# Optimization experiments

Measured on AMD Instinct MI355X. Metric: run time of the kernel, lower is better.

Reference implementation:

```python
import jax, jax.numpy as jnp
import numpy as np

N_NODES = 50000
N_EDGES = 800000
D = 64
N_LAYERS = 5
N_GRAPHS = 256
N_CLASSES = 10
BN_EPS = 1e-5


def setup_inputs() -> dict:
    key = jax.random.key(0)
    ks = jax.random.split(key, 16)
    s = 1.0 / np.sqrt(D)
    return {
        "X": jax.random.normal(ks[0], (N_NODES, D), jnp.float32),
        "edge_index": jax.random.randint(ks[1], (2, N_EDGES), 0, N_NODES, jnp.int64),
        "batch": jnp.sort(jax.random.randint(ks[2], (N_NODES,), 0, N_GRAPHS, jnp.int64)),
        "Wk": jax.random.normal(ks[3], (N_LAYERS, D, D), jnp.float32) * s,
        "Wq": jax.random.normal(ks[4], (N_LAYERS, D, D), jnp.float32) * s,
        "Wv": jax.random.normal(ks[5], (N_LAYERS, D, D), jnp.float32) * s,
        "Ws": jax.random.normal(ks[6], (N_LAYERS, D, D), jnp.float32) * s,
        "bk": jnp.zeros((N_LAYERS, D), jnp.float32),
        "bq": jnp.zeros((N_LAYERS, D), jnp.float32),
        "bv": jnp.zeros((N_LAYERS, D), jnp.float32),
        "bconv": jnp.zeros((N_LAYERS, D), jnp.float32),
        "gamma": jnp.ones((N_LAYERS, D), jnp.float32),
        "beta": jnp.zeros((N_LAYERS, D), jnp.float32),
        "Wlin": jax.random.normal(ks[7], (D, N_CLASSES), jnp.float32) * s,
        "blin": jnp.zeros((N_CLASSES,), jnp.float32),
    }


def _res_gated_conv(x, src, dst, Wk, Wq, Wv, Ws, bk, bq, bv, b):
    # PyG ResGatedGraphConv: out_i = W_skip x_i + b + sum_{j->i} sigmoid(K x_i + Q x_j) * (V x_j)
    k = x @ Wk + bk  # [N, D]
    q = x @ Wq + bq
    v = x @ Wv + bv
    eta = jax.nn.sigmoid(k[dst] + q[src])         # [E, D] gate
    agg = jax.ops.segment_sum(eta * v[src], dst, num_segments=x.shape[0])
    return agg + x @ Ws + b


def _batch_norm(x, gamma, beta):
    mean = jnp.mean(x, axis=0)
    var = jnp.mean(jnp.square(x - mean), axis=0)  # biased, as torch BN training
    return (x - mean) * jax.lax.rsqrt(var + BN_EPS) * gamma + beta


def reference(X, edge_index, batch, Wk, Wq, Wv, Ws, bk, bq, bv, bconv, gamma, beta, Wlin, blin):
    src, dst = edge_index[0], edge_index[1]
    h = X
    for l in range(N_LAYERS):  # dropout_prob = 0 -> dropout is identity
        h = _res_gated_conv(h, src, dst, Wk[l], Wq[l], Wv[l], Ws[l], bk[l], bq[l], bv[l], bconv[l])
        h = jax.nn.relu(h)
        h = _batch_norm(h, gamma[l], beta[l])
    # global mean pool over graphs
    sums = jax.ops.segment_sum(h, batch, num_segments=N_GRAPHS)
    counts = jax.ops.segment_sum(jnp.ones((h.shape[0], 1), h.dtype), batch, num_segments=N_GRAPHS)
    pooled = sums / jnp.maximum(counts, 1.0)
    logits = pooled @ Wlin + blin
    return jax.nn.softmax(logits, axis=-1)
```

## Files before the change

### kernel.cpp

```cpp
#include <hip/hip_runtime.h>

#define NN 50000
#define NE 800000
#define DD 64
#define NL 5
#define NG 256
#define NC 10
#define BN_EPS 1e-5f
#define NCHUNK ((NN + 255) / 256)
#define GROWS 64
#define GT (GROWS / 16)
#define SAW 68
#define GEMM_BLOCKS ((NN + GROWS - 1) / GROWS)
#define NNS (NN + 8)
#define PADDEG(d) (((d) + 7) & ~7)
#define DEG_BLOCKS ((NE + 255) / 256)
#define WPREP_BLOCKS ((NL * 2048 + 255) / 256)
#define FCHK 2048
#define FCHUNKS ((NE + FCHK - 1) / FCHK)
#define FILLP_BLOCKS (8 * FCHUNKS)
#define NRANGE (NN / 8)
#define PAD_BLOCKS NCHUNK
#define L2E 1.4426950408889634f

typedef __attribute__((ext_vector_type(8))) short bf16x8;
typedef __attribute__((ext_vector_type(4))) float f32x4;

__device__ inline float bf2f(unsigned short u) {
    return __uint_as_float((unsigned)u << 16);
}
__device__ inline unsigned short f2bf(float x) {
    unsigned u = __float_as_uint(x);
    u += 0x7FFFu + ((u >> 16) & 1u);
    return (unsigned short)(u >> 16);
}

__device__ inline unsigned int pack_bf16x2(float a, float b) {
    unsigned int ua = __float_as_uint(a);
    unsigned int ub = __float_as_uint(b);
    ua += 0x7FFFu + ((ua >> 16) & 1u);
    ub += 0x7FFFu + ((ub >> 16) & 1u);
    return (ub & 0xFFFF0000u) | (ua >> 16);
}

__device__ inline void split_bf16(float x, short& h, short& l) {
    const unsigned u  = __float_as_uint(x);
    const unsigned hb = u & 0xFFFF0000u;
    h = (short)(hb >> 16);
    const float lo = x - __uint_as_float(hb);
    l = (short)(__float_as_uint(lo) >> 16);
}

__device__ inline float p_eq(unsigned p) { return __uint_as_float(p << 16); }
__device__ inline float p_v(unsigned p)  { return __uint_as_float(p & 0xFFFF0000u); }

#define GPAIR(ek, pa, pb, acc) { \
    const float t1_ = fmaf(ek, p_eq(pa), 1.f); \
    const float t2_ = fmaf(ek, p_eq(pb), 1.f); \
    const float R_  = __builtin_amdgcn_rcpf(t1_ * t2_); \
    acc = fmaf(fmaf(p_v(pb), t1_, p_v(pa) * t2_), R_, acc); }

#define GCOLS(ekx, eky, p, accx, accy) { \
    const float t1_ = fmaf(ekx, p_eq(p.x), 1.f); \
    const float t2_ = fmaf(eky, p_eq(p.y), 1.f); \
    const float R_  = __builtin_amdgcn_rcpf(t1_ * t2_); \
    accx = fmaf(p_v(p.x), R_ * t2_, accx); \
    accy = fmaf(p_v(p.y), R_ * t1_, accy); }

template<int F32>
__device__ __forceinline__ void gemm_body(
    const void* __restrict__ HinV,
    const bf16x8* __restrict__ whbuf, const bf16x8* __restrict__ wlbuf,
    const float* __restrict__ bk, const float* __restrict__ bq,
    const float* __restrict__ bv, const float* __restrict__ bs,
    const float* __restrict__ prevStats,
    const float* __restrict__ prevGamma, const float* __restrict__ prevBeta,
    unsigned short* __restrict__ Kq, unsigned int* __restrict__ QVq,
    unsigned short* __restrict__ Hq, const int gb)
{
    __shared__ unsigned int sA[GROWS * SAW];
    __shared__ float sAB[128];
    const int tid = threadIdx.x;

    if (!F32) {
        if (tid < 64) {
            const float invN = 1.0f / (float)NN;
            const float mean = prevStats[tid] * invN;
            const float var  = prevStats[64 + tid] * invN - mean * mean;
            const float inv  = rsqrtf(var + BN_EPS);
            const float a = inv * prevGamma[tid];
            sAB[tid]      = a;
            sAB[64 + tid] = prevBeta[tid] - mean * a;
        }
        __syncthreads();
    }

    const int row0 = gb * GROWS;
    if (F32) {
        const float* X = (const float*)HinV;
        for (int i = tid; i < GROWS * 16; i += 256) {
            const int row = i >> 4;
            const int k4  = (i & 15) * 4;
            float4 x = make_float4(0.f, 0.f, 0.f, 0.f);
            if (row0 + row < NN)
                x = *(const float4*)(X + (size_t)(row0 + row) * DD + k4);
            const float xs[4] = {x.x, x.y, x.z, x.w};
            unsigned int* dst = &sA[row * SAW + k4];
#pragma unroll
            for (int j = 0; j < 4; j++) {
                short hs, ls;
                split_bf16(xs[j], hs, ls);
                dst[j] = ((unsigned int)(unsigned short)hs << 16) | (unsigned short)ls;
            }
        }
    } else {
        const unsigned short* Hin = (const unsigned short*)HinV;
        for (int i = tid; i < GROWS * 8; i += 256) {
            const int row = i >> 3;
            const int cb  = (i & 7) * 8;
            const int q   = cb >> 4;
            const int o16 = cb & 15;
            uint4 v = make_uint4(0u, 0u, 0u, 0u);
            if (row0 + row < NN)
                v = *(const uint4*)&Hin[((size_t)q * NN + row0 + row) * 16 + o16];
            const unsigned ws[4] = {v.x, v.y, v.z, v.w};
            unsigned int* dst = &sA[row * SAW + cb];
#pragma unroll
            for (int j = 0; j < 4; j++) {
                const float x0 = bf2f((unsigned short)(ws[j] & 0xFFFFu));
                const float x1 = bf2f((unsigned short)(ws[j] >> 16));
                const int c0 = cb + 2 * j, c1 = cb + 2 * j + 1;
                short hs, ls;
                split_bf16(fmaf(x0, sAB[c0], sAB[64 + c0]), hs, ls);
                dst[2 * j] = ((unsigned int)(unsigned short)hs << 16) | (unsigned short)ls;
                split_bf16(fmaf(x1, sAB[c1], sAB[64 + c1]), hs, ls);
                dst[2 * j + 1] = ((unsigned int)(unsigned short)hs << 16) | (unsigned short)ls;
            }
        }
    }

    const int wave = tid >> 6;
    const int lane = tid & 63;
    const int n15  = lane & 15;
    const int g    = lane >> 4;
    const int col  = wave * 16 + n15;

    bf16x8 wh[4][2], wl[4][2];
    {
        const int base = wave * 64 + lane;
#pragma unroll
        for (int m = 0; m < 4; m++)
#pragma unroll
            for (int c = 0; c < 2; c++) {
                const int idx = m * 512 + c * 256 + base;
                wh[m][c] = whbuf[idx];
                wl[m][c] = wlbuf[idx];
            }
    }

    const float nbk = -bk[col] * L2E;
    const float nbq = -bq[col] * L2E;
    const float bvc = bv[col], bsc = bs[col];
    __syncthreads();

#pragma unroll 1
    for (int t = 0; t < GT; t++) {
        const int rowbase = row0 + t * 16;
        if (rowbase >= NN) break;

        bf16x8 ah[2], al[2];
#pragma unroll
        for (int c = 0; c < 2; c++) {
            const uint4 u0 = *(const uint4*)&sA[(t * 16 + n15) * SAW + g * 8 + 32 * c];
            const uint4 u1 = *(const uint4*)&sA[(t * 16 + n15) * SAW + g * 8 + 32 * c + 4];
            const unsigned int us[8] = {u0.x, u0.y, u0.z, u0.w, u1.x, u1.y, u1.z, u1.w};
            bf16x8 h, l;
#pragma unroll
            for (int j = 0; j < 8; j++) {
                h[j] = (short)(us[j] >> 16);
                l[j] = (short)(us[j] & 0xFFFFu);
            }
            ah[c] = h; al[c] = l;
        }

        f32x4 acc[4];
#pragma unroll
        for (int m = 0; m < 4; m++) acc[m] = (f32x4){0.f, 0.f, 0.f, 0.f};

#pragma unroll
        for (int c = 0; c < 2; c++) {
#pragma unroll
            for (int m = 0; m < 4; m++) {
                acc[m] = __builtin_amdgcn_mfma_f32_16x16x32_bf16(ah[c], wh[m][c], acc[m], 0, 0, 0);
                acc[m] = __builtin_amdgcn_mfma_f32_16x16x32_bf16(al[c], wh[m][c], acc[m], 0, 0, 0);
                acc[m] = __builtin_amdgcn_mfma_f32_16x16x32_bf16(ah[c], wl[m][c], acc[m], 0, 0, 0);
            }
        }

#pragma unroll
        for (int r = 0; r < 4; r++) {
            const int row = rowbase + g * 4 + r;
            const size_t o  = ((size_t)wave * NN  + row) * 16 + n15;
            const size_t oq = ((size_t)wave * NNS + row) * 16 + n15;
            Kq[o]   = f2bf(__builtin_amdgcn_exp2f(fmaf(acc[0][r], -L2E, nbk)));
            QVq[oq] = pack_bf16x2(__builtin_amdgcn_exp2f(fmaf(acc[1][r], -L2E, nbq)),
                                  acc[2][r] + bvc);
            Hq[o]   = f2bf(acc[3][r] + bsc);
        }
    }
}

__global__ __launch_bounds__(256) void prep_kernel(
    const int* __restrict__ ei, int* __restrict__ deg,
    const float* __restrict__ Wk, const float* __restrict__ Wq,
    const float* __restrict__ Wv, const float* __restrict__ Ws,
    bf16x8* __restrict__ whbuf, bf16x8* __restrict__ wlbuf,
    unsigned int* __restrict__ QVq)
{
    const int bid = blockIdx.x;
    if (bid < DEG_BLOCKS) {
        const int e = bid * 256 + threadIdx.x;
        if (e < NE) atomicAdd(&deg[ei[NE + e]], 1);
        return;
    }
    if (bid == DEG_BLOCKS && threadIdx.x < 64) {
        const int q = threadIdx.x >> 4, c = threadIdx.x & 15;
        QVq[((size_t)q * NNS + NN) * 16 + c] = 0u;
    }
    const int t = (bid - DEG_BLOCKS) * 256 + threadIdx.x;
    if (t >= NL * 2048) return;
    const int lane = t & 63;
    const int w    = (t >> 6) & 3;
    const int c    = (t >> 8) & 1;
    const int m    = (t >> 9) & 3;
    const int l    = t >> 11;

    const float* Wm4[4] = {Wk, Wq, Wv, Ws};
    const float* W = Wm4[m] + l * 4096;
    const int col = w * 16 + (lane & 15);
    const int g   = lane >> 4;

    bf16x8 h, lo;
#pragma unroll
    for (int j = 0; j < 8; j++) {
        const int k = g * 8 + j + 32 * c;
        short hs, ls;
        split_bf16(W[k * DD + col], hs, ls);
        h[j] = hs; lo[j] = ls;
    }
    whbuf[t] = h;
    wlbuf[t] = lo;
}

__global__ __launch_bounds__(256) void scan_partial_kernel(
    const int* __restrict__ deg, int* __restrict__ psums)
{
    __shared__ int ls[256];
    const int i = blockIdx.x * 256 + threadIdx.x;
    ls[threadIdx.x] = (i < NN) ? PADDEG(deg[i]) : 0;
    __syncthreads();
    for (int off = 128; off > 0; off >>= 1) {
        if (threadIdx.x < off) ls[threadIdx.x] += ls[threadIdx.x + off];
        __syncthreads();
    }
    if (threadIdx.x == 0) psums[blockIdx.x] = ls[0];
}

__global__ __launch_bounds__(64) void scan_offsets_kernel(
    int* __restrict__ psums, int* __restrict__ rowst)
{
    const int lane = threadIdx.x;
    const int base = lane * 4;
    int v[4];
    int s = 0;
#pragma unroll
    for (int j = 0; j < 4; j++) {
        v[j] = (base + j < NCHUNK) ? psums[base + j] : 0;
        s += v[j];
    }
    int incl = s;
    for (int off = 1; off < 64; off <<= 1) {
        const int t = __shfl_up(incl, off);
        if (lane >= off) incl += t;
    }
    const int total = __shfl(incl, 63);
    int run = incl - s;
#pragma unroll
    for (int j = 0; j < 4; j++) {
        if (base + j < NCHUNK) psums[base + j] = run;
        run += v[j];
    }
    if (lane == 0) rowst[NN] = total;
}

__global__ __launch_bounds__(256) void scan_final_kernel(
    const int* __restrict__ deg, const int* __restrict__ psums,
    int* __restrict__ rowst, int* __restrict__ cursor)
{
    __shared__ int ls[256];
    const int i = blockIdx.x * 256 + threadIdx.x;
    const int x = (i < NN) ? PADDEG(deg[i]) : 0;
    ls[threadIdx.x] = x;
    __syncthreads();
    for (int off = 1; off < 256; off <<= 1) {
        int v = (threadIdx.x >= off) ? ls[threadIdx.x - off] : 0;
        __syncthreads();
        ls[threadIdx.x] += v;
        __syncthreads();
    }
    if (i < NN) {
        const int excl = psums[blockIdx.x] + ls[threadIdx.x] - x;
        rowst[i]  = excl;
        cursor[i] = excl;
    }
}

__global__ __launch_bounds__(256) void gfp_kernel(
    const float* __restrict__ X,
    const bf16x8* __restrict__ whbuf, const bf16x8* __restrict__ wlbuf,
    const float* __restrict__ bk, const float* __restrict__ bq,
    const float* __restrict__ bv, const float* __restrict__ bs,
    unsigned short* __restrict__ Kq, unsigned int* __restrict__ QVq,
    unsigned short* __restrict__ Hq,
    const int* __restrict__ ei, int* __restrict__ cursor,
    const int* __restrict__ rowst, const int* __restrict__ deg,
    unsigned short* __restrict__ csr16)
{
    const int bid = blockIdx.x;
    if (bid < GEMM_BLOCKS) {
        gemm_body<1>(X, whbuf, wlbuf, bk, bq, bv, bs,
                     nullptr, nullptr, nullptr, Kq, QVq, Hq, bid);
        return;
    }
    if (bid < GEMM_BLOCKS + FILLP_BLOCKS) {
        const int fid = bid - GEMM_BLOCKS;
        const int r   = bid & 7;
        const int o   = fid >> 3;
        const int lo  = r * NRANGE;
        const int hi  = lo + NRANGE;
        const int e0  = o * FCHK;
        const int e1  = min(e0 + FCHK, NE);
        for (int e = e0 + threadIdx.x; e < e1; e += 256) {
            const int dst = ei[NE + e];
            if (dst >= lo && dst < hi) {
                const int src = ei[e];
                csr16[atomicAdd(&cursor[dst], 1)] = (unsigned short)src;
            }
        }
        return;
    }
    const int n = (bid - GEMM_BLOCKS - FILLP_BLOCKS) * 256 + threadIdx.x;
    if (n >= NN) return;
    const int end = rowst[n + 1];
    for (int i = rowst[n] + deg[n]; i < end; i++) csr16[i] = (unsigned short)NN;
}

__global__ __launch_bounds__(256) void gemm4_mfma(
    const void* __restrict__ HinV,
    const bf16x8* __restrict__ whbuf, const bf16x8* __restrict__ wlbuf,
    const float* __restrict__ bk, const float* __restrict__ bq,
    const float* __restrict__ bv, const float* __restrict__ bs,
    const float* __restrict__ prevStats,
    const float* __restrict__ prevGamma, const float* __restrict__ prevBeta,
    unsigned short* __restrict__ Kq, unsigned int* __restrict__ QVq,
    unsigned short* __restrict__ Hq)
{
    gemm_body<0>(HinV, whbuf, wlbuf, bk, bq, bv, bs,
                 prevStats, prevGamma, prevBeta, Kq, QVq, Hq, blockIdx.x);
}

#define GATHER_BLOCKS (8 * 782)
__global__ __launch_bounds__(256) void gather_kernel(
    const int* __restrict__ rowst, const unsigned short* __restrict__ csr16,
    const unsigned short* __restrict__ Kq, const unsigned int* __restrict__ QVq,
    unsigned short* Hq, float* __restrict__ stats)
{
    const int tid  = threadIdx.x;
    const int wv   = tid >> 6;
    const int lane = tid & 63;
    const int eoff = lane >> 3;
    const int cp   = lane & 7;

    const int j       = blockIdx.x;
    const int xcd     = j & 7;
    const int quarter = xcd >> 1;
    const int half    = xcd & 1;
    const int nodebase = ((j >> 3) * 2 + half) * 32 + wv * 8;

    const unsigned* Kq32 = (const unsigned*)(Kq + (size_t)quarter * NN * 16);
    const uint2*    Qq2  = (const uint2*)(QVq + (size_t)quarter * NNS * 16);
    unsigned*       Hq32 = (unsigned*)(Hq + (size_t)quarter * NN * 16);

    float se = 0.f, s2e = 0.f, so = 0.f, s2o = 0.f;

    int e00 = __builtin_amdgcn_readfirstlane(rowst[min(nodebase, NN)]);

    for (int t = 0; t < 4; t++) {
        const int n0 = nodebase + 2 * t;
        if (n0 >= NN) break;
        const int n1 = n0 + 1;
        const unsigned ho0 = (unsigned)(n0 * 8 + cp);
        const unsigned ho1 = (unsigned)(n1 * 8 + cp);
        unsigned h0p = 0u, h1p = 0u;
        if (eoff == 0) {
            h0p = Hq32[ho0];
            h1p = Hq32[ho1];
        }
        const unsigned k0p = Kq32[ho0];
        const unsigned k1p = Kq32[ho1];
        const float ek00 = bf2f((unsigned short)(k0p & 0xFFFFu));
        const float ek01 = bf2f((unsigned short)(k0p >> 16));
        const float ek10 = bf2f((unsigned short)(k1p & 0xFFFFu));
        const float ek11 = bf2f((unsigned short)(k1p >> 16));
        const int e01 = __builtin_amdgcn_readfirstlane(rowst[n1]);
        const int e11 = __builtin_amdgcn_readfirstlane(rowst[n1 + 1]);
        int nd0 = (e01 - e00) >> 3;
        int nd1 = (e11 - e01) >> 3;
        int ndm = min(nd0, nd1);
        nd0 -= ndm; nd1 -= ndm;
        int b0 = e00, b1 = e01;
        e00 = e11;
        float a00 = 0.f, a01 = 0.f, a10 = 0.f, a11 = 0.f;

        while (ndm >= 2) {
            const unsigned s0 = *(const unsigned*)(csr16 + b0 + 2 * eoff);
            const unsigned s1 = *(const unsigned*)(csr16 + b1 + 2 * eoff);
            const uint2 p0a = Qq2[(s0 & 0xFFFFu) * 8u + cp];
            const uint2 p0b = Qq2[(s0 >> 16) * 8u + cp];
            const uint2 p1a = Qq2[(s1 & 0xFFFFu) * 8u + cp];
            const uint2 p1b = Qq2[(s1 >> 16) * 8u + cp];
            GPAIR(ek00, p0a.x, p0b.x, a00);
            GPAIR(ek01, p0a.y, p0b.y, a01);
            GPAIR(ek10, p1a.x, p1b.x, a10);
            GPAIR(ek11, p1a.y, p1b.y, a11);
            b0 += 16; b1 += 16; ndm -= 2;
        }
        if (ndm) {
            const int s0 = csr16[b0 + eoff];
            const int s1 = csr16[b1 + eoff];
            const uint2 p0 = Qq2[(unsigned)(s0 * 8 + cp)];
            const uint2 p1 = Qq2[(unsigned)(s1 * 8 + cp)];
            GCOLS(ek00, ek01, p0, a00, a01);
            GCOLS(ek10, ek11, p1, a10, a11);
            b0 += 8; b1 += 8;
        }
        while (nd0 >= 2) {
            const unsigned s0 = *(const unsigned*)(csr16 + b0 + 2 * eoff);
            const uint2 p0a = Qq2[(s0 & 0xFFFFu) * 8u + cp];
            const uint2 p0b = Qq2[(s0 >> 16) * 8u + cp];
            GPAIR(ek00, p0a.x, p0b.x, a00);
            GPAIR(ek01, p0a.y, p0b.y, a01);
            b0 += 16; nd0 -= 2;
        }
        if (nd0) {
            const int s0 = csr16[b0 + eoff];
            const uint2 p0 = Qq2[(unsigned)(s0 * 8 + cp)];
            GCOLS(ek00, ek01, p0, a00, a01);
        }
        while (nd1 >= 2) {
            const unsigned s1 = *(const unsigned*)(csr16 + b1 + 2 * eoff);
            const uint2 p1a = Qq2[(s1 & 0xFFFFu) * 8u + cp];
            const uint2 p1b = Qq2[(s1 >> 16) * 8u + cp];
            GPAIR(ek10, p1a.x, p1b.x, a10);
            GPAIR(ek11, p1a.y, p1b.y, a11);
            b1 += 16; nd1 -= 2;
        }
        if (nd1) {
            const int s1 = csr16[b1 + eoff];
            const uint2 p1 = Qq2[(unsigned)(s1 * 8 + cp)];
            GCOLS(ek10, ek11, p1, a10, a11);
        }

        a00 += __shfl_xor(a00, 8);  a00 += __shfl_xor(a00, 16); a00 += __shfl_xor(a00, 32);
        a01 += __shfl_xor(a01, 8);  a01 += __shfl_xor(a01, 16); a01 += __shfl_xor(a01, 32);
        a10 += __shfl_xor(a10, 8);  a10 += __shfl_xor(a10, 16); a10 += __shfl_xor(a10, 32);
        a11 += __shfl_xor(a11, 8);  a11 += __shfl_xor(a11, 16); a11 += __shfl_xor(a11, 32);

        if (eoff == 0) {
            const float o00 = fmaxf(bf2f((unsigned short)(h0p & 0xFFFFu)) + a00, 0.f);
            const float o01 = fmaxf(bf2f((unsigned short)(h0p >> 16))     + a01, 0.f);
            const float o10 = fmaxf(bf2f((unsigned short)(h1p & 0xFFFFu)) + a10, 0.f);
            const float o11 = fmaxf(bf2f((unsigned short)(h1p >> 16))     + a11, 0.f);
            const unsigned short b00 = f2bf(o00), b01 = f2bf(o01);
            const unsigned short b10 = f2bf(o10), b11 = f2bf(o11);
            Hq32[ho0] = ((unsigned)b01 << 16) | b00;
            Hq32[ho1] = ((unsigned)b11 << 16) | b10;
            const float r00 = bf2f(b00), r01 = bf2f(b01);
            const float r10 = bf2f(b10), r11 = bf2f(b11);
            se  += r00 + r10;  s2e += r00 * r00 + r10 * r10;
            so  += r01 + r11;  s2o += r01 * r01 + r11 * r11;
        }
    }

    __shared__ float ls[64], ls2[64];
    if (eoff == 0) {
        ls[wv * 16 + 2 * cp]      = se;  ls2[wv * 16 + 2 * cp]      = s2e;
        ls[wv * 16 + 2 * cp + 1]  = so;  ls2[wv * 16 + 2 * cp + 1]  = s2o;
    }
    __syncthreads();
    if (tid < 16) {
        const float a = ls[tid] + ls[16 + tid] + ls[32 + tid] + ls[48 + tid];
        const float b = ls2[tid] + ls2[16 + tid] + ls2[32 + tid] + ls2[48 + tid];
        atomicAdd(&stats[quarter * 16 + tid], a);
        atomicAdd(&stats[64 + quarter * 16 + tid], b);
    }
}

#define POOL_ROWS 64
__global__ __launch_bounds__(256) void pool_kernel(
    const unsigned short* __restrict__ Hq, const int* __restrict__ batch,
    float* __restrict__ psum, float* __restrict__ pcnt)
{
    const int sub = threadIdx.x >> 5;
    const int c   = threadIdx.x & 31;
    const int q   = c >> 3;
    const int p   = c & 7;
    const int r0 = (blockIdx.x * 8 + sub) * POOL_ROWS;
    if (r0 >= NN) return;
    const int r1 = min(r0 + POOL_ROWS, NN);
    const unsigned* Hqq = (const unsigned*)(Hq + (size_t)q * NN * 16);
    const int col0 = q * 16 + 2 * p;

    int cur = batch[r0];
    float acc0 = 0.f, acc1 = 0.f, cnt = 0.f;
    for (int r = r0; r < r1; r++) {
        const int g = batch[r];
        if (g != cur) {
            atomicAdd(&psum[cur * DD + col0], acc0);
            atomicAdd(&psum[cur * DD + col0 + 1], acc1);
            if (c == 0) atomicAdd(&pcnt[cur], cnt);
            acc0 = 0.f; acc1 = 0.f; cnt = 0.f; cur = g;
        }
        const unsigned hv = Hqq[(size_t)r * 8 + p];
        acc0 += bf2f((unsigned short)(hv & 0xFFFFu));
        acc1 += bf2f((unsigned short)(hv >> 16));
        cnt += 1.f;
    }
    atomicAdd(&psum[cur * DD + col0], acc0);
    atomicAdd(&psum[cur * DD + col0 + 1], acc1);
    if (c == 0) atomicAdd(&pcnt[cur], cnt);
}

__global__ __launch_bounds__(256) void final_kernel(
    const float* __restrict__ psum, const float* __restrict__ pcnt,
    const float* __restrict__ stats,
    const float* __restrict__ gamma, const float* __restrict__ beta,
    const float* __restrict__ Wlin, const float* __restrict__ blin,
    float* __restrict__ out)
{
    const int g = blockIdx.x * blockDim.x + threadIdx.x;
    if (g >= NG) return;

    const float invc = 1.0f / fmaxf(pcnt[g], 1.0f);
    const float invN = 1.0f / (float)NN;
    float p[DD];
#pragma unroll
    for (int d = 0; d < DD; d++) {
        const float mean = stats[d] * invN;
        const float var  = stats[64 + d] * invN - mean * mean;
        const float inv  = rsqrtf(var + BN_EPS);
        const float a = inv * gamma[d];
        const float b = beta[d] - mean * a;
        p[d] = fmaf(psum[g * DD + d] * invc, a, b);
    }

    float logits[NC];
    float m = -1e30f;
#pragma unroll
    for (int c = 0; c < NC; c++) {
        float acc = blin[c];
#pragma unroll
        for (int d = 0; d < DD; d++) acc = fmaf(p[d], Wlin[d * NC + c], acc);
        logits[c] = acc;
        m = fmaxf(m, acc);
    }
    float sum = 0.f;
#pragma unroll
    for (int c = 0; c < NC; c++) {
        logits[c] = __expf(logits[c] - m);
        sum += logits[c];
    }
    const float inv = 1.f / sum;
#pragma unroll
    for (int c = 0; c < NC; c++) out[g * NC + c] = logits[c] * inv;
}

extern "C" void kernel_launch(void* const* d_in, const int* in_sizes, int n_in,
                              void* d_out, int out_size, void* d_ws, size_t ws_size,
                              hipStream_t stream)
{
    const float* X     = (const float*)d_in[0];
    const int*   ei    = (const int*)d_in[1];
    const int*   batch = (const int*)d_in[2];
    const float* Wk    = (const float*)d_in[3];
    const float* Wq    = (const float*)d_in[4];
    const float* Wv    = (const float*)d_in[5];
    const float* Ws    = (const float*)d_in[6];
    const float* bk    = (const float*)d_in[7];
    const float* bq    = (const float*)d_in[8];
    const float* bv    = (const float*)d_in[9];
    const float* bconv = (const float*)d_in[10];
    const float* gamma = (const float*)d_in[11];
    const float* beta  = (const float*)d_in[12];
    const float* Wlin  = (const float*)d_in[13];
    const float* blin  = (const float*)d_in[14];
    float* out = (float*)d_out;

    const size_t M  = (size_t)NN * DD;
    const size_t MQ = (size_t)4 * NNS * 16;
    unsigned short* Kq  = (unsigned short*)d_ws;
    unsigned int*   QVq = (unsigned int*)(Kq + M);
    unsigned short* H0q = (unsigned short*)(QVq + MQ);
    unsigned short* H1q = H0q + M;
    int*   deg   = (int*)(H1q + M);
    float* psum  = (float*)(deg + NN);
    float* pcnt  = psum + (size_t)NG * DD;
    float* stats = pcnt + NG;
    int* rowst  = (int*)(stats + NL * 128);
    int* cursor = rowst + NN + 1;
    int* psums  = cursor + NN;
    unsigned short* csr16 = (unsigned short*)(psums + 256);
    bf16x8* whbuf = (bf16x8*)(csr16 + NE + 8 * NN);
    bf16x8* wlbuf = whbuf + NL * 2048;

    const size_t zero_bytes = (size_t)(NN + NG * DD + NG + NL * 128) * sizeof(float);
    hipMemsetAsync(deg, 0, zero_bytes, stream);

    prep_kernel<<<DEG_BLOCKS + WPREP_BLOCKS, 256, 0, stream>>>(
        ei, deg, Wk, Wq, Wv, Ws, whbuf, wlbuf, QVq);

    scan_partial_kernel<<<NCHUNK, 256, 0, stream>>>(deg, psums);
    scan_offsets_kernel<<<1, 64, 0, stream>>>(psums, rowst);
    scan_final_kernel<<<NCHUNK, 256, 0, stream>>>(deg, psums, rowst, cursor);

    gfp_kernel<<<GEMM_BLOCKS + FILLP_BLOCKS + PAD_BLOCKS, 256, 0, stream>>>(
        X, whbuf, wlbuf, bk, bq, bv, bconv,
        Kq, QVq, H0q, ei, cursor, rowst, deg, csr16);

    gather_kernel<<<GATHER_BLOCKS, 256, 0, stream>>>(
        rowst, csr16, Kq, QVq, H0q, stats);
    const void* hin = (const void*)H0q;
    for (int l = 1; l < NL; l++) {
        unsigned short* hout = (l & 1) ? H1q : H0q;
        gemm4_mfma<<<GEMM_BLOCKS, 256, 0, stream>>>(
            hin, whbuf + l * 2048, wlbuf + l * 2048,
            bk + l * 64, bq + l * 64, bv + l * 64, bconv + l * 64,
            stats + (l - 1) * 128, gamma + (l - 1) * 64, beta + (l - 1) * 64,
            Kq, QVq, hout);
        gather_kernel<<<GATHER_BLOCKS, 256, 0, stream>>>(
            rowst, csr16, Kq, QVq, hout, stats + l * 128);
        hin = (const void*)hout;
    }

    pool_kernel<<<(NN + 8 * POOL_ROWS - 1) / (8 * POOL_ROWS), 256, 0, stream>>>(
        (const unsigned short*)hin, batch, psum, pcnt);
    final_kernel<<<1, 256, 0, stream>>>(
        psum, pcnt, stats + 4 * 128, gamma + 4 * 64, beta + 4 * 64, Wlin, blin, out);
}
```

Before: 533.8 us.

## Prefetch next CSR index in gather loops, double GEMM tile rows

The edge aggregation loops now software-pipeline the CSR neighbour-index load, fetching the next pair of source indices before the current gather, so the dependent index-then-Q load chain overlaps. The readfirstlane hints on row-start loads are dropped, which may move those values from scalar to vector registers. The GEMM row tile grows from 64 to 128 rows, halving the block count and doubling shared memory per block, which can lower occupancy.

```diff
diff --git a/kernel.cpp b/kernel.cpp
--- a/kernel.cpp
+++ b/kernel.cpp
@@ -8,7 +8,7 @@
 #define NC 10
 #define BN_EPS 1e-5f
 #define NCHUNK ((NN + 255) / 256)
-#define GROWS 64
+#define GROWS 128
 #define GT (GROWS / 16)
 #define SAW 68
 #define GEMM_BLOCKS ((NN + GROWS - 1) / GROWS)
@@ -67,6 +67,16 @@
     accx = fmaf(p_v(p.x), R_ * t2_, accx); \
     accy = fmaf(p_v(p.y), R_ * t1_, accy); }
 
+#define GBODY4(s0, s1) { \
+    const uint2 p0a = Qq2[((s0) & 0xFFFFu) * 8u + cp]; \
+    const uint2 p0b = Qq2[((s0) >> 16) * 8u + cp]; \
+    const uint2 p1a = Qq2[((s1) & 0xFFFFu) * 8u + cp]; \
+    const uint2 p1b = Qq2[((s1) >> 16) * 8u + cp]; \
+    GPAIR(ek00, p0a.x, p0b.x, a00); \
+    GPAIR(ek01, p0a.y, p0b.y, a01); \
+    GPAIR(ek10, p1a.x, p1b.x, a10); \
+    GPAIR(ek11, p1a.y, p1b.y, a11); }
+
 template<int F32>
 __device__ __forceinline__ void gemm_body(
     const void* __restrict__ HinV,
@@ -393,7 +403,7 @@
 
     float se = 0.f, s2e = 0.f, so = 0.f, s2o = 0.f;
 
-    int e00 = __builtin_amdgcn_readfirstlane(rowst[min(nodebase, NN)]);
+    int e00 = rowst[min(nodebase, NN)];
 
     for (int t = 0; t < 4; t++) {
         const int n0 = nodebase + 2 * t;
@@ -412,8 +422,7 @@
         const float ek01 = bf2f((unsigned short)(k0p >> 16));
         const float ek10 = bf2f((unsigned short)(k1p & 0xFFFFu));
         const float ek11 = bf2f((unsigned short)(k1p >> 16));
-        const int e01 = __builtin_amdgcn_readfirstlane(rowst[n1]);
-        const int e11 = __builtin_amdgcn_readfirstlane(rowst[n1 + 1]);
+        const int e01 = rowst[n1], e11 = rowst[n1 + 1];
         int nd0 = (e01 - e00) >> 3;
         int nd1 = (e11 - e01) >> 3;
         int ndm = min(nd0, nd1);
@@ -422,17 +431,17 @@
         e00 = e11;
         float a00 = 0.f, a01 = 0.f, a10 = 0.f, a11 = 0.f;
 
-        while (ndm >= 2) {
-            const unsigned s0 = *(const unsigned*)(csr16 + b0 + 2 * eoff);
-            const unsigned s1 = *(const unsigned*)(csr16 + b1 + 2 * eoff);
-            const uint2 p0a = Qq2[(s0 & 0xFFFFu) * 8u + cp];
-            const uint2 p0b = Qq2[(s0 >> 16) * 8u + cp];
-            const uint2 p1a = Qq2[(s1 & 0xFFFFu) * 8u + cp];
-            const uint2 p1b = Qq2[(s1 >> 16) * 8u + cp];
-            GPAIR(ek00, p0a.x, p0b.x, a00);
-            GPAIR(ek01, p0a.y, p0b.y, a01);
-            GPAIR(ek10, p1a.x, p1b.x, a10);
-            GPAIR(ek11, p1a.y, p1b.y, a11);
+        if (ndm >= 2) {
+            unsigned s0 = *(const unsigned*)(csr16 + b0 + 2 * eoff);
+            unsigned s1 = *(const unsigned*)(csr16 + b1 + 2 * eoff);
+            while (ndm >= 4) {
+                const unsigned s0n = *(const unsigned*)(csr16 + b0 + 16 + 2 * eoff);
+                const unsigned s1n = *(const unsigned*)(csr16 + b1 + 16 + 2 * eoff);
+                GBODY4(s0, s1);
+                s0 = s0n; s1 = s1n;
+                b0 += 16; b1 += 16; ndm -= 2;
+            }
+            GBODY4(s0, s1);
             b0 += 16; b1 += 16; ndm -= 2;
         }
         if (ndm) {
@@ -444,8 +453,16 @@
             GCOLS(ek10, ek11, p1, a10, a11);
             b0 += 8; b1 += 8;
         }
-        while (nd0 >= 2) {
-            const unsigned s0 = *(const unsigned*)(csr16 + b0 + 2 * eoff);
+        if (nd0 >= 2) {
+            unsigned s0 = *(const unsigned*)(csr16 + b0 + 2 * eoff);
+            while (nd0 >= 4) {
+                const unsigned s0n = *(const unsigned*)(csr16 + b0 + 16 + 2 * eoff);
+                const uint2 p0a = Qq2[(s0 & 0xFFFFu) * 8u + cp];
+                const uint2 p0b = Qq2[(s0 >> 16) * 8u + cp];
+                GPAIR(ek00, p0a.x, p0b.x, a00);
+                GPAIR(ek01, p0a.y, p0b.y, a01);
+                s0 = s0n; b0 += 16; nd0 -= 2;
+            }
             const uint2 p0a = Qq2[(s0 & 0xFFFFu) * 8u + cp];
             const uint2 p0b = Qq2[(s0 >> 16) * 8u + cp];
             GPAIR(ek00, p0a.x, p0b.x, a00);
@@ -457,8 +474,16 @@
             const uint2 p0 = Qq2[(unsigned)(s0 * 8 + cp)];
             GCOLS(ek00, ek01, p0, a00, a01);
         }
-        while (nd1 >= 2) {
-            const unsigned s1 = *(const unsigned*)(csr16 + b1 + 2 * eoff);
+        if (nd1 >= 2) {
+            unsigned s1 = *(const unsigned*)(csr16 + b1 + 2 * eoff);
+            while (nd1 >= 4) {
+                const unsigned s1n = *(const unsigned*)(csr16 + b1 + 16 + 2 * eoff);
+                const uint2 p1a = Qq2[(s1 & 0xFFFFu) * 8u + cp];
+                const uint2 p1b = Qq2[(s1 >> 16) * 8u + cp];
+                GPAIR(ek10, p1a.x, p1b.x, a10);
+                GPAIR(ek11, p1a.y, p1b.y, a11);
+                s1 = s1n; b1 += 16; nd1 -= 2;
+            }
             const uint2 p1a = Qq2[(s1 & 0xFFFFu) * 8u + cp];
             const uint2 p1b = Qq2[(s1 >> 16) * 8u + cp];
             GPAIR(ek10, p1a.x, p1b.x, a10);
```

New measurement: 543.9 us. About the same (+1.9%).

## Fold scan-offsets and final kernels into last-block tails, enlarge GEMM tile rows

Applied to the files above, without the earlier changes.

Merges the single-block scan_offsets kernel into scan_partial and the final softmax kernel into pool_kernel using atomic ticket counters, so the last block to finish does the tail work. This removes two kernel launches and their dependency gaps. It also doubles GROWS to 128 rows per GEMM block, which halves the GEMM block count and may change occupancy and the GEMM tiling. It also replaces readfirstlane on the rowst loads with plain loads. The ticket scheme adds atomics and fences, and it relies on the ticket counters being zeroed by the memset.

```diff
diff --git a/kernel.cpp b/kernel.cpp
--- a/kernel.cpp
+++ b/kernel.cpp
@@ -8,7 +8,7 @@
 #define NC 10
 #define BN_EPS 1e-5f
 #define NCHUNK ((NN + 255) / 256)
-#define GROWS 64
+#define GROWS 128
 #define GT (GROWS / 16)
 #define SAW 68
 #define GEMM_BLOCKS ((NN + GROWS - 1) / GROWS)
@@ -21,6 +21,8 @@
 #define FILLP_BLOCKS (8 * FCHUNKS)
 #define NRANGE (NN / 8)
 #define PAD_BLOCKS NCHUNK
+#define POOL_ROWS 64
+#define POOL_BLOCKS ((NN + 8 * POOL_ROWS - 1) / (8 * POOL_ROWS))
 #define L2E 1.4426950408889634f
 
 typedef __attribute__((ext_vector_type(8))) short bf16x8;
@@ -253,9 +255,11 @@
 }
 
 __global__ __launch_bounds__(256) void scan_partial_kernel(
-    const int* __restrict__ deg, int* __restrict__ psums)
+    const int* __restrict__ deg, int* __restrict__ psums,
+    int* __restrict__ rowst, int* __restrict__ ticket)
 {
     __shared__ int ls[256];
+    __shared__ int amLast;
     const int i = blockIdx.x * 256 + threadIdx.x;
     ls[threadIdx.x] = (i < NN) ? PADDEG(deg[i]) : 0;
     __syncthreads();
@@ -263,19 +267,21 @@
         if (threadIdx.x < off) ls[threadIdx.x] += ls[threadIdx.x + off];
         __syncthreads();
     }
-    if (threadIdx.x == 0) psums[blockIdx.x] = ls[0];
-}
-
-__global__ __launch_bounds__(64) void scan_offsets_kernel(
-    int* __restrict__ psums, int* __restrict__ rowst)
-{
+    if (threadIdx.x == 0) {
+        atomicExch(&psums[blockIdx.x], ls[0]);
+        __threadfence();
+        amLast = (atomicAdd(ticket, 1) == NCHUNK - 1);
+    }
+    __syncthreads();
+    if (!amLast || threadIdx.x >= 64) return;
+
     const int lane = threadIdx.x;
     const int base = lane * 4;
     int v[4];
     int s = 0;
 #pragma unroll
     for (int j = 0; j < 4; j++) {
-        v[j] = (base + j < NCHUNK) ? psums[base + j] : 0;
+        v[j] = (base + j < NCHUNK) ? atomicAdd(&psums[base + j], 0) : 0;
         s += v[j];
     }
     int incl = s;
@@ -393,7 +399,7 @@
 
     float se = 0.f, s2e = 0.f, so = 0.f, s2o = 0.f;
 
-    int e00 = __builtin_amdgcn_readfirstlane(rowst[min(nodebase, NN)]);
+    int e00 = rowst[min(nodebase, NN)];
 
     for (int t = 0; t < 4; t++) {
         const int n0 = nodebase + 2 * t;
@@ -412,8 +418,7 @@
         const float ek01 = bf2f((unsigned short)(k0p >> 16));
         const float ek10 = bf2f((unsigned short)(k1p & 0xFFFFu));
         const float ek11 = bf2f((unsigned short)(k1p >> 16));
-        const int e01 = __builtin_amdgcn_readfirstlane(rowst[n1]);
-        const int e11 = __builtin_amdgcn_readfirstlane(rowst[n1 + 1]);
+        const int e01 = rowst[n1], e11 = rowst[n1 + 1];
         int nd0 = (e01 - e00) >> 3;
         int nd1 = (e11 - e01) >> 3;
         int ndm = min(nd0, nd1);
@@ -506,54 +511,57 @@
     }
 }
 
-#define POOL_ROWS 64
 __global__ __launch_bounds__(256) void pool_kernel(
     const unsigned short* __restrict__ Hq, const int* __restrict__ batch,
-    float* __restrict__ psum, float* __restrict__ pcnt)
+    float* __restrict__ psum, float* __restrict__ pcnt, int* __restrict__ ticket,
+    const float* __restrict__ stats,
+    const float* __restrict__ gamma, const float* __restrict__ beta,
+    const float* __restrict__ Wlin, const float* __restrict__ blin,
+    float* __restrict__ out)
 {
     const int sub = threadIdx.x >> 5;
     const int c   = threadIdx.x & 31;
     const int q   = c >> 3;
     const int p   = c & 7;
     const int r0 = (blockIdx.x * 8 + sub) * POOL_ROWS;
-    if (r0 >= NN) return;
-    const int r1 = min(r0 + POOL_ROWS, NN);
-    const unsigned* Hqq = (const unsigned*)(Hq + (size_t)q * NN * 16);
-    const int col0 = q * 16 + 2 * p;
-
-    int cur = batch[r0];
-    float acc0 = 0.f, acc1 = 0.f, cnt = 0.f;
-    for (int r = r0; r < r1; r++) {
-        const int g = batch[r];
-        if (g != cur) {
-            atomicAdd(&psum[cur * DD + col0], acc0);
-            atomicAdd(&psum[cur * DD + col0 + 1], acc1);
-            if (c == 0) atomicAdd(&pcnt[cur], cnt);
-            acc0 = 0.f; acc1 = 0.f; cnt = 0.f; cur = g;
-        }
-        const unsigned hv = Hqq[(size_t)r * 8 + p];
-        acc0 += bf2f((unsigned short)(hv & 0xFFFFu));
-        acc1 += bf2f((unsigned short)(hv >> 16));
-        cnt += 1.f;
-    }
-    atomicAdd(&psum[cur * DD + col0], acc0);
-    atomicAdd(&psum[cur * DD + col0 + 1], acc1);
-    if (c == 0) atomicAdd(&pcnt[cur], cnt);
-}
-
-__global__ __launch_bounds__(256) void final_kernel(
-    const float* __restrict__ psum, const float* __restrict__ pcnt,
-    const float* __restrict__ stats,
-    const float* __restrict__ gamma, const float* __restrict__ beta,
-    const float* __restrict__ Wlin, const float* __restrict__ blin,
-    float* __restrict__ out)
-{
-    const int g = blockIdx.x * blockDim.x + threadIdx.x;
-    if (g >= NG) return;
-
-    const float invc = 1.0f / fmaxf(pcnt[g], 1.0f);
+    if (r0 < NN) {
+        const int r1 = min(r0 + POOL_ROWS, NN);
+        const unsigned* Hqq = (const unsigned*)(Hq + (size_t)q * NN * 16);
+        const int col0 = q * 16 + 2 * p;
+
+        int cur = batch[r0];
+        float acc0 = 0.f, acc1 = 0.f, cnt = 0.f;
+        for (int r = r0; r < r1; r++) {
+            const int g = batch[r];
+            if (g != cur) {
+                atomicAdd(&psum[cur * DD + col0], acc0);
+                atomicAdd(&psum[cur * DD + col0 + 1], acc1);
+                if (c == 0) atomicAdd(&pcnt[cur], cnt);
+                acc0 = 0.f; acc1 = 0.f; cnt = 0.f; cur = g;
+            }
+            const unsigned hv = Hqq[(size_t)r * 8 + p];
+            acc0 += bf2f((unsigned short)(hv & 0xFFFFu));
+            acc1 += bf2f((unsigned short)(hv >> 16));
+            cnt += 1.f;
+        }
+        atomicAdd(&psum[cur * DD + col0], acc0);
+        atomicAdd(&psum[cur * DD + col0 + 1], acc1);
+        if (c == 0) atomicAdd(&pcnt[cur], cnt);
+    }
+
+    __shared__ int amLast;
+    __syncthreads();
+    if (threadIdx.x == 0) {
+        __threadfence();
+        amLast = (atomicAdd(ticket, 1) == POOL_BLOCKS - 1);
+    }
+    __syncthreads();
+    if (!amLast) return;
+
+    const int g = threadIdx.x;
+    const float invc = 1.0f / fmaxf(atomicAdd(&pcnt[g], 0.f), 1.0f);
     const float invN = 1.0f / (float)NN;
-    float p[DD];
+    float pv[DD];
 #pragma unroll
     for (int d = 0; d < DD; d++) {
         const float mean = stats[d] * invN;
@@ -561,28 +569,28 @@
         const float inv  = rsqrtf(var + BN_EPS);
         const float a = inv * gamma[d];
         const float b = beta[d] - mean * a;
-        p[d] = fmaf(psum[g * DD + d] * invc, a, b);
+        pv[d] = fmaf(atomicAdd(&psum[g * DD + d], 0.f) * invc, a, b);
     }
 
     float logits[NC];
     float m = -1e30f;
 #pragma unroll
-    for (int c = 0; c < NC; c++) {
-        float acc = blin[c];
-#pragma unroll
-        for (int d = 0; d < DD; d++) acc = fmaf(p[d], Wlin[d * NC + c], acc);
-        logits[c] = acc;
+    for (int cc = 0; cc < NC; cc++) {
+        float acc = blin[cc];
+#pragma unroll
+        for (int d = 0; d < DD; d++) acc = fmaf(pv[d], Wlin[d * NC + cc], acc);
+        logits[cc] = acc;
         m = fmaxf(m, acc);
     }
     float sum = 0.f;
 #pragma unroll
-    for (int c = 0; c < NC; c++) {
-        logits[c] = __expf(logits[c] - m);
-        sum += logits[c];
+    for (int cc = 0; cc < NC; cc++) {
+        logits[cc] = __expf(logits[cc] - m);
+        sum += logits[cc];
     }
     const float inv = 1.f / sum;
 #pragma unroll
-    for (int c = 0; c < NC; c++) out[g * NC + c] = logits[c] * inv;
+    for (int cc = 0; cc < NC; cc++) out[g * NC + cc] = logits[cc] * inv;
 }
 
 extern "C" void kernel_launch(void* const* d_in, const int* in_sizes, int n_in,
@@ -612,25 +620,25 @@
     unsigned int*   QVq = (unsigned int*)(Kq + M);
     unsigned short* H0q = (unsigned short*)(QVq + MQ);
     unsigned short* H1q = H0q + M;
-    int*   deg   = (int*)(H1q + M);
-    float* psum  = (float*)(deg + NN);
-    float* pcnt  = psum + (size_t)NG * DD;
-    float* stats = pcnt + NG;
-    int* rowst  = (int*)(stats + NL * 128);
+    int*   deg    = (int*)(H1q + M);
+    float* psum   = (float*)(deg + NN);
+    float* pcnt   = psum + (size_t)NG * DD;
+    float* stats  = pcnt + NG;
+    int*   ticket = (int*)(stats + NL * 128);
+    int* rowst  = ticket + 2;
     int* cursor = rowst + NN + 1;
     int* psums  = cursor + NN;
     unsigned short* csr16 = (unsigned short*)(psums + 256);
     bf16x8* whbuf = (bf16x8*)(csr16 + NE + 8 * NN);
     bf16x8* wlbuf = whbuf + NL * 2048;
 
-    const size_t zero_bytes = (size_t)(NN + NG * DD + NG + NL * 128) * sizeof(float);
+    const size_t zero_bytes = (size_t)(NN + NG * DD + NG + NL * 128 + 2) * 4;
     hipMemsetAsync(deg, 0, zero_bytes, stream);
 
     prep_kernel<<<DEG_BLOCKS + WPREP_BLOCKS, 256, 0, stream>>>(
         ei, deg, Wk, Wq, Wv, Ws, whbuf, wlbuf, QVq);
 
-    scan_partial_kernel<<<NCHUNK, 256, 0, stream>>>(deg, psums);
-    scan_offsets_kernel<<<1, 64, 0, stream>>>(psums, rowst);
+    scan_partial_kernel<<<NCHUNK, 256, 0, stream>>>(deg, psums, rowst, ticket);
     scan_final_kernel<<<NCHUNK, 256, 0, stream>>>(deg, psums, rowst, cursor);
 
     gfp_kernel<<<GEMM_BLOCKS + FILLP_BLOCKS + PAD_BLOCKS, 256, 0, stream>>>(
@@ -652,8 +660,7 @@
         hin = (const void*)hout;
     }
 
-    pool_kernel<<<(NN + 8 * POOL_ROWS - 1) / (8 * POOL_ROWS), 256, 0, stream>>>(
-        (const unsigned short*)hin, batch, psum, pcnt);
-    final_kernel<<<1, 256, 0, stream>>>(
-        psum, pcnt, stats + 4 * 128, gamma + 4 * 64, beta + 4 * 64, Wlin, blin, out);
-}
+    pool_kernel<<<POOL_BLOCKS, 256, 0, stream>>>(
+        (const unsigned short*)hin, batch, psum, pcnt, ticket + 1,
+        stats + 4 * 128, gamma + 4 * 64, beta + 4 * 64, Wlin, blin, out);
+}
```

Measured after the change: 551.9 us. 3.4% more time.

## Replicate BN stats accumulators, double GEMM tile rows, drop readfirstlane

Applied to the files above, without the earlier changes.

Spreads the per-layer batch-norm sum and sum-of-squares atomics across four replicated stat slots, chosen by block index. The goal is less atomic contention on the same addresses. Consumers (the next GEMM and the final kernel) now sum the four replicas. GROWS is also raised from 64 to 128 rows per GEMM block, halving the block count. The readfirstlane hints on rowst loads are removed, which may leave those values in vector registers instead of scalar ones.

```diff
diff --git a/kernel.cpp b/kernel.cpp
--- a/kernel.cpp
+++ b/kernel.cpp
@@ -8,7 +8,7 @@
 #define NC 10
 #define BN_EPS 1e-5f
 #define NCHUNK ((NN + 255) / 256)
-#define GROWS 64
+#define GROWS 128
 #define GT (GROWS / 16)
 #define SAW 68
 #define GEMM_BLOCKS ((NN + GROWS - 1) / GROWS)
@@ -21,6 +21,8 @@
 #define FILLP_BLOCKS (8 * FCHUNKS)
 #define NRANGE (NN / 8)
 #define PAD_BLOCKS NCHUNK
+#define SREP 4
+#define SSTR (SREP * 128)
 #define L2E 1.4426950408889634f
 
 typedef __attribute__((ext_vector_type(8))) short bf16x8;
@@ -84,9 +86,15 @@
 
     if (!F32) {
         if (tid < 64) {
+            float s1 = 0.f, s2 = 0.f;
+#pragma unroll
+            for (int r = 0; r < SREP; r++) {
+                s1 += prevStats[r * 128 + tid];
+                s2 += prevStats[r * 128 + 64 + tid];
+            }
             const float invN = 1.0f / (float)NN;
-            const float mean = prevStats[tid] * invN;
-            const float var  = prevStats[64 + tid] * invN - mean * mean;
+            const float mean = s1 * invN;
+            const float var  = s2 * invN - mean * mean;
             const float inv  = rsqrtf(var + BN_EPS);
             const float a = inv * prevGamma[tid];
             sAB[tid]      = a;
@@ -393,7 +401,7 @@
 
     float se = 0.f, s2e = 0.f, so = 0.f, s2o = 0.f;
 
-    int e00 = __builtin_amdgcn_readfirstlane(rowst[min(nodebase, NN)]);
+    int e00 = rowst[min(nodebase, NN)];
 
     for (int t = 0; t < 4; t++) {
         const int n0 = nodebase + 2 * t;
@@ -412,8 +420,7 @@
         const float ek01 = bf2f((unsigned short)(k0p >> 16));
         const float ek10 = bf2f((unsigned short)(k1p & 0xFFFFu));
         const float ek11 = bf2f((unsigned short)(k1p >> 16));
-        const int e01 = __builtin_amdgcn_readfirstlane(rowst[n1]);
-        const int e11 = __builtin_amdgcn_readfirstlane(rowst[n1 + 1]);
+        const int e01 = rowst[n1], e11 = rowst[n1 + 1];
         int nd0 = (e01 - e00) >> 3;
         int nd1 = (e11 - e01) >> 3;
         int ndm = min(nd0, nd1);
@@ -499,10 +506,11 @@
     }
     __syncthreads();
     if (tid < 16) {
+        const int rep = (j >> 3) & (SREP - 1);
         const float a = ls[tid] + ls[16 + tid] + ls[32 + tid] + ls[48 + tid];
         const float b = ls2[tid] + ls2[16 + tid] + ls2[32 + tid] + ls2[48 + tid];
-        atomicAdd(&stats[quarter * 16 + tid], a);
-        atomicAdd(&stats[64 + quarter * 16 + tid], b);
+        atomicAdd(&stats[rep * 128 + quarter * 16 + tid], a);
+        atomicAdd(&stats[rep * 128 + 64 + quarter * 16 + tid], b);
     }
 }
 
@@ -556,8 +564,14 @@
     float p[DD];
 #pragma unroll
     for (int d = 0; d < DD; d++) {
-        const float mean = stats[d] * invN;
-        const float var  = stats[64 + d] * invN - mean * mean;
+        float s1 = 0.f, s2 = 0.f;
+#pragma unroll
+        for (int r = 0; r < SREP; r++) {
+            s1 += stats[r * 128 + d];
+            s2 += stats[r * 128 + 64 + d];
+        }
+        const float mean = s1 * invN;
+        const float var  = s2 * invN - mean * mean;
         const float inv  = rsqrtf(var + BN_EPS);
         const float a = inv * gamma[d];
         const float b = beta[d] - mean * a;
@@ -616,14 +630,14 @@
     float* psum  = (float*)(deg + NN);
     float* pcnt  = psum + (size_t)NG * DD;
     float* stats = pcnt + NG;
-    int* rowst  = (int*)(stats + NL * 128);
+    int* rowst  = (int*)(stats + NL * SSTR);
     int* cursor = rowst + NN + 1;
     int* psums  = cursor + NN;
     unsigned short* csr16 = (unsigned short*)(psums + 256);
     bf16x8* whbuf = (bf16x8*)(csr16 + NE + 8 * NN);
     bf16x8* wlbuf = whbuf + NL * 2048;
 
-    const size_t zero_bytes = (size_t)(NN + NG * DD + NG + NL * 128) * sizeof(float);
+    const size_t zero_bytes = (size_t)(NN + NG * DD + NG + NL * SSTR) * 4;
     hipMemsetAsync(deg, 0, zero_bytes, stream);
 
     prep_kernel<<<DEG_BLOCKS + WPREP_BLOCKS, 256, 0, stream>>>(
@@ -645,15 +659,15 @@
         gemm4_mfma<<<GEMM_BLOCKS, 256, 0, stream>>>(
             hin, whbuf + l * 2048, wlbuf + l * 2048,
             bk + l * 64, bq + l * 64, bv + l * 64, bconv + l * 64,
-            stats + (l - 1) * 128, gamma + (l - 1) * 64, beta + (l - 1) * 64,
+            stats + (l - 1) * SSTR, gamma + (l - 1) * 64, beta + (l - 1) * 64,
             Kq, QVq, hout);
         gather_kernel<<<GATHER_BLOCKS, 256, 0, stream>>>(
-            rowst, csr16, Kq, QVq, hout, stats + l * 128);
+            rowst, csr16, Kq, QVq, hout, stats + l * SSTR);
         hin = (const void*)hout;
     }
 
     pool_kernel<<<(NN + 8 * POOL_ROWS - 1) / (8 * POOL_ROWS), 256, 0, stream>>>(
         (const unsigned short*)hin, batch, psum, pcnt);
     final_kernel<<<1, 256, 0, stream>>>(
-        psum, pcnt, stats + 4 * 128, gamma + 4 * 64, beta + 4 * 64, Wlin, blin, out);
-}
+        psum, pcnt, stats + 4 * SSTR, gamma + 4 * 64, beta + 4 * 64, Wlin, blin, out);
+}
```

Result: faster. 518.5 us (-2.9%).
